# Optimization experiments

Hardware: AMD Instinct MI355X
Metric: run time of the kernel (lower is better)

Reference implementation:

```python
import jax, jax.numpy as jnp
import numpy as np

NUM_HEADS = 16
HEAD_DIM = 128
D_MODEL = 2048
SEQ = 2048
BATCH = 1


def setup_inputs() -> dict:
    key = jax.random.key(0)
    ks = jax.random.split(key, 7)
    s = 0.02
    return {
        "x": jax.random.normal(ks[0], (BATCH, SEQ, D_MODEL), dtype=jnp.float32),
        "q_w": jax.random.normal(ks[1], (D_MODEL, D_MODEL), dtype=jnp.float32) * s,
        "k_w": jax.random.normal(ks[2], (D_MODEL, D_MODEL), dtype=jnp.float32) * s,
        "v_w": jax.random.normal(ks[3], (D_MODEL, D_MODEL), dtype=jnp.float32) * s,
        "o_w": jax.random.normal(ks[4], (D_MODEL, D_MODEL), dtype=jnp.float32) * s,
        "gate_w": jax.random.normal(ks[5], (HEAD_DIM, HEAD_DIM), dtype=jnp.float32) * s,
        "gate_b": jax.random.normal(ks[6], (HEAD_DIM,), dtype=jnp.float32) * s,
    }


def reference(x, q_w, k_w, v_w, o_w, gate_w, gate_b):
    B, S, D = x.shape
    H, Hd = NUM_HEADS, HEAD_DIM
    # QKV projections (nn.Linear: y = x @ W^T), split into heads -> [B,H,S,Hd]
    def proj(w):
        return jnp.einsum('bsd,ed->bse', x, w).reshape(B, S, H, Hd).transpose(0, 2, 1, 3)
    q = proj(q_w)
    k = proj(k_w)
    v = proj(v_w)
    scale = 1.0 / jnp.sqrt(jnp.asarray(Hd, dtype=x.dtype))
    scores = jnp.einsum('bhqd,bhkd->bhqk', q, k) * scale  # [B,H,S,S]
    # causal mask
    causal = jnp.tril(jnp.ones((S, S), dtype=bool))
    scores = jnp.where(causal, scores, jnp.asarray(-1e30, dtype=scores.dtype))
    attn = jax.nn.softmax(scores, axis=-1)
    av = jnp.einsum('bhqk,bhkd->bhqd', attn, v)  # [B,H,S,Hd]
    # learned sigmoid gate computed from q, applied elementwise to attention output
    gate = jax.nn.sigmoid(jnp.einsum('bhqd,ed->bhqe', q, gate_w) + gate_b)
    out = av * gate
    out = out.transpose(0, 2, 1, 3).reshape(B, S, D)
    return jnp.einsum('bsd,ed->bse', out, o_w)
```

## Files before the change

### kernel.cpp

```cpp
#include <hip/hip_runtime.h>
#include <stdint.h>
#include <math.h>

#define DM 2048
#define NH 16
#define HD 128
#define LDQ (3 * DM)

typedef __bf16 bf16;
typedef __attribute__((ext_vector_type(8))) __bf16 bf16x8;
typedef __attribute__((ext_vector_type(4))) float f32x4;
typedef __attribute__((ext_vector_type(2))) unsigned int u32x2;

__device__ __forceinline__ void gload_lds16(const void* g, void* l) {
  __builtin_amdgcn_global_load_lds(
      (const __attribute__((address_space(1))) void*)g,
      (__attribute__((address_space(3))) void*)l,
      16, 0, 0);
}

__device__ __forceinline__ unsigned lds_addr(const void* p) {
  return (unsigned)(size_t)(const __attribute__((address_space(3))) void*)p;
}

template <int OFF>
__device__ __forceinline__ u32x2 tr_read(unsigned va) {
  u32x2 r;
  asm volatile("ds_read_b64_tr_b16 %0, %1 offset:%2"
               : "=v"(r) : "v"(va), "i"(OFF));
  return r;
}

#define TR4(dst, vd)                                        \
  dst[0] = tr_read<0>(vd);   dst[1] = tr_read<512>(vd);     \
  dst[2] = tr_read<1024>(vd); dst[3] = tr_read<1536>(vd);

__global__ __launch_bounds__(256) void cvt6(const float* xs, const float* qws,
                                            const float* kws, const float* vws,
                                            const float* ows, const float* gws,
                                            ushort* xd, ushort* w3d, ushort* owd,
                                            ushort* gwd) {
  const int y = blockIdx.y;
  const float4* s; ushort4* d; int n = (DM * DM) / 4;
  switch (y) {
    case 0: s = (const float4*)xs;  d = (ushort4*)xd;  break;
    case 1: s = (const float4*)qws; d = (ushort4*)w3d; break;
    case 2: s = (const float4*)kws; d = (ushort4*)(w3d + (size_t)DM * DM); break;
    case 3: s = (const float4*)vws; d = (ushort4*)(w3d + (size_t)2 * DM * DM); break;
    case 4: s = (const float4*)ows; d = (ushort4*)owd; break;
    default: s = (const float4*)gws; d = (ushort4*)gwd; n = (HD * HD) / 4; break;
  }
  int i = blockIdx.x * 256 + threadIdx.x;
  if (i >= n) return;
  float4 v = s[i];
  union { bf16 b[4]; ushort4 u; } r;
  r.b[0] = (bf16)v.x; r.b[1] = (bf16)v.y; r.b[2] = (bf16)v.z; r.b[3] = (bf16)v.w;
  d[i] = r.u;
}

__global__ __launch_bounds__(512, 2) void gemm_qkv(const bf16* __restrict__ A,
                                                   const bf16* __restrict__ Bw,
                                                   bf16* __restrict__ C) {
  __shared__ __align__(16) bf16 LA[2][256 * 64];
  __shared__ __align__(16) bf16 LB[2][192 * 64];
  const int tid = threadIdx.x;
  const int w = tid >> 6, l = tid & 63;
  const int wm = w >> 2, wn = w & 3;
  const int fr = l & 15, fg = l >> 4;
  const int bid = blockIdx.x;
  const int xcd = bid & 7, idx = bid >> 3;
  const int bm0 = (idx >> 2) * 256;
  const int bn0 = ((xcd << 2) | (idx & 3)) * 192;

  const int srow = l >> 3;
  const int sunit = (l & 7) ^ srow;
  const bf16* pa = A + (size_t)(bm0 + w * 32 + srow) * DM + sunit * 8;
  const bf16* pb = Bw + (size_t)(bn0 + w * 24 + srow) * DM + sunit * 8;

#define STG(buf, kt)                                                        \
  {                                                                         \
    _Pragma("unroll")                                                       \
    for (int i = 0; i < 4; i++)                                             \
      gload_lds16(pa + (size_t)i * 8 * DM + (kt) * 64,                      \
                  &LA[buf][(w * 32 + i * 8) * 64]);                         \
    _Pragma("unroll")                                                       \
    for (int i = 0; i < 3; i++)                                             \
      gload_lds16(pb + (size_t)i * 8 * DM + (kt) * 64,                      \
                  &LB[buf][(w * 24 + i * 8) * 64]);                         \
  }

  f32x4 acc[8][3] = {};

  STG(0, 0);
  STG(1, 1);
  asm volatile("s_waitcnt vmcnt(7)" ::: "memory");
  __builtin_amdgcn_s_barrier();

  const int sw0 = ((fg) ^ (fr & 7)) << 4;
  const int sw1 = ((4 + fg) ^ (fr & 7)) << 4;
  const char* AB = (const char*)&LA[0][0];
  const char* BB = (const char*)&LB[0][0];
  const int aoff = (wm * 128 + fr) * 128;
  const int boff = (wn * 48 + fr) * 128;

  bf16x8 bA[3], bB[3], aP[4], aQ[4], aR[4], aS[4];

#pragma unroll
  for (int n = 0; n < 3; n++) bA[n] = *(const bf16x8*)(BB + boff + n * 2048 + sw0);
#pragma unroll
  for (int m = 0; m < 4; m++) aP[m] = *(const bf16x8*)(AB + aoff + m * 2048 + sw0);
#pragma unroll
  for (int m = 0; m < 4; m++) aQ[m] = *(const bf16x8*)(AB + aoff + (m + 4) * 2048 + sw0);
  __builtin_amdgcn_sched_barrier(0);

  for (int t = 0; t < 32; ++t) {
    const int cur = t & 1;
    const char* Ac = AB + cur * 32768;
    const char* Bc = BB + cur * 24576;
#pragma unroll
    for (int n = 0; n < 3; n++) bB[n] = *(const bf16x8*)(Bc + boff + n * 2048 + sw1);
#pragma unroll
    for (int m = 0; m < 4; m++) aR[m] = *(const bf16x8*)(Ac + aoff + m * 2048 + sw1);
    asm volatile("s_waitcnt lgkmcnt(11)" ::: "memory");
    __builtin_amdgcn_sched_barrier(0);
    __builtin_amdgcn_s_setprio(1);
#pragma unroll
    for (int m = 0; m < 4; m++)
#pragma unroll
      for (int n = 0; n < 3; n++)
        acc[m][n] = __builtin_amdgcn_mfma_f32_16x16x32_bf16(aP[m], bA[n], acc[m][n], 0, 0, 0);
    __builtin_amdgcn_s_setprio(0);
    __builtin_amdgcn_sched_barrier(0);
#pragma unroll
    for (int m = 0; m < 4; m++) aS[m] = *(const bf16x8*)(Ac + aoff + (m + 4) * 2048 + sw1);
    asm volatile("s_waitcnt lgkmcnt(11)" ::: "memory");
    __builtin_amdgcn_sched_barrier(0);
    __builtin_amdgcn_s_setprio(1);
#pragma unroll
    for (int m = 0; m < 4; m++)
#pragma unroll
      for (int n = 0; n < 3; n++)
        acc[m + 4][n] = __builtin_amdgcn_mfma_f32_16x16x32_bf16(aQ[m], bA[n], acc[m + 4][n], 0, 0, 0);
    __builtin_amdgcn_s_setprio(0);
    __builtin_amdgcn_sched_barrier(0);
    asm volatile("s_waitcnt lgkmcnt(4)" ::: "memory");
    __builtin_amdgcn_sched_barrier(0);
    __builtin_amdgcn_s_setprio(1);
#pragma unroll
    for (int m = 0; m < 4; m++)
#pragma unroll
      for (int n = 0; n < 3; n++)
        acc[m][n] = __builtin_amdgcn_mfma_f32_16x16x32_bf16(aR[m], bB[n], acc[m][n], 0, 0, 0);
    __builtin_amdgcn_s_setprio(0);
    __builtin_amdgcn_sched_barrier(0);
    asm volatile("s_waitcnt lgkmcnt(0)" ::: "memory");
    __builtin_amdgcn_sched_barrier(0);
    __builtin_amdgcn_s_setprio(1);
#pragma unroll
    for (int m = 0; m < 4; m++)
#pragma unroll
      for (int n = 0; n < 3; n++)
        acc[m + 4][n] = __builtin_amdgcn_mfma_f32_16x16x32_bf16(aS[m], bB[n], acc[m + 4][n], 0, 0, 0);
    __builtin_amdgcn_s_setprio(0);
    __builtin_amdgcn_sched_barrier(0);

    __builtin_amdgcn_s_barrier();
    if (t < 30) {
      STG(cur, t + 2);
      asm volatile("s_waitcnt vmcnt(7)" ::: "memory");
    } else {
      asm volatile("s_waitcnt vmcnt(0)" ::: "memory");
    }
    __builtin_amdgcn_s_barrier();
    if (t < 31) {
      const char* An = AB + (cur ^ 1) * 32768;
      const char* Bn = BB + (cur ^ 1) * 24576;
#pragma unroll
      for (int n = 0; n < 3; n++) bA[n] = *(const bf16x8*)(Bn + boff + n * 2048 + sw0);
#pragma unroll
      for (int m = 0; m < 4; m++) aP[m] = *(const bf16x8*)(An + aoff + m * 2048 + sw0);
#pragma unroll
      for (int m = 0; m < 4; m++) aQ[m] = *(const bf16x8*)(An + aoff + (m + 4) * 2048 + sw0);
    }
    __builtin_amdgcn_sched_barrier(0);
  }

#pragma unroll
  for (int m = 0; m < 8; m++) {
    const int row0 = bm0 + wm * 128 + m * 16 + fg * 4;
#pragma unroll
    for (int n = 0; n < 3; n++) {
      const int col = bn0 + wn * 48 + n * 16 + fr;
#pragma unroll
      for (int j = 0; j < 4; j++) C[(size_t)(row0 + j) * LDQ + col] = (bf16)acc[m][n][j];
    }
  }
#undef STG
}

template <typename OutT>
__global__ __launch_bounds__(256) void gemm128(const bf16* __restrict__ A,
                                               const bf16* __restrict__ Bw,
                                               OutT* __restrict__ C, int ldc) {
  __shared__ __align__(16) bf16 As[128 * 32];
  __shared__ __align__(16) bf16 Bs[128 * 32];
  const int tid = threadIdx.x;
  const int w = tid >> 6, l = tid & 63;
  const int wr = w >> 1, wc = w & 1;
  const int bx = blockIdx.x, by = blockIdx.y;
  const int lrow = l >> 2, lcol = (l & 3) * 8;
  const int fr = l & 15, fg = l >> 4;
  const bf16* Ag = A + (size_t)(by * 128 + w * 32 + lrow) * DM + lcol;
  const bf16* Bg = Bw + (size_t)(bx * 128 + w * 32 + lrow) * DM + lcol;
  bf16* Asw = &As[(w * 32) * 32];
  bf16* Bsw = &Bs[(w * 32) * 32];
  f32x4 acc[4][4] = {};
  for (int kt = 0; kt < DM / 32; ++kt) {
    const int ko = kt * 32;
    gload_lds16(Ag + ko, Asw);
    gload_lds16(Ag + ko + 16 * DM, Asw + 16 * 32);
    gload_lds16(Bg + ko, Bsw);
    gload_lds16(Bg + ko + 16 * DM, Bsw + 16 * 32);
    __syncthreads();
    bf16x8 af[4], bfr[4];
#pragma unroll
    for (int m = 0; m < 4; m++)
      af[m] = *(const bf16x8*)&As[(wr * 64 + m * 16 + fr) * 32 + fg * 8];
#pragma unroll
    for (int n = 0; n < 4; n++)
      bfr[n] = *(const bf16x8*)&Bs[(wc * 64 + n * 16 + fr) * 32 + fg * 8];
#pragma unroll
    for (int m = 0; m < 4; m++)
#pragma unroll
      for (int n = 0; n < 4; n++)
        acc[m][n] = __builtin_amdgcn_mfma_f32_16x16x32_bf16(af[m], bfr[n], acc[m][n], 0, 0, 0);
    __syncthreads();
  }
#pragma unroll
  for (int m = 0; m < 4; m++) {
    const int row0 = by * 128 + wr * 64 + m * 16 + fg * 4;
#pragma unroll
    for (int n = 0; n < 4; n++) {
      const int col = bx * 128 + wc * 64 + n * 16 + fr;
#pragma unroll
      for (int j = 0; j < 4; j++) C[(size_t)(row0 + j) * ldc + col] = (OutT)acc[m][n][j];
    }
  }
}

__global__ __launch_bounds__(256, 2) void attn_k(const bf16* __restrict__ QKV,
                                                 const bf16* __restrict__ GWb,
                                                 const float* __restrict__ gbias,
                                                 bf16* __restrict__ Gout) {
  __shared__ __align__(16) bf16 Ks[2][8192];
  __shared__ __align__(16) bf16 Vs[2][8192];
  const int gid = blockIdx.x;
  const int h = gid & 15;
  const int idx = gid >> 4;
  const int qt = (idx < 16) ? (31 - idx) : (idx - 16);
  const int tid = threadIdx.x;
  const int w = tid >> 6, l = tid & 63;
  const int fr = l & 15, fg = l >> 4;
  const int fg4 = fg * 4;
  const int qbase = qt * 64 + w * 16;
  const int qg = qbase + fr;
  const int qcol = h * HD;
  const int kcol = DM + h * HD;
  const int vcol = 2 * DM + h * HD;
  const float scale = 0.08838834764831845f;

  bf16x8 bq[4];
#pragma unroll
  for (int kt = 0; kt < 4; kt++)
    bq[kt] = *(const bf16x8*)&QKV[(size_t)(qbase + fr) * LDQ + qcol + kt * 32 + fg * 8];

  const bf16* vbase = QKV + (size_t)(l >> 1) * LDQ + vcol + (l & 1) * 8;
  bf16* Ksl = &Ks[0][0];
  bf16* Vsl = &Vs[0][0];
  const unsigned ldsb = lds_addr(Vsl) + 8u * (unsigned)l;

#define STAGE(buf, kvbase)                                                    \
  {                                                                           \
    _Pragma("unroll")                                                         \
    for (int c = 0; c < 4; c++) {                                             \
      const int i = w * 4 + c;                                                \
      const int krow = i * 4 + (l >> 4);                                      \
      const int c16 = (l & 15) ^ (krow & 7);                                  \
      gload_lds16(QKV + (size_t)((kvbase) + krow) * LDQ + kcol + c16 * 8,     \
                  Ksl + (buf) * 8192 + i * 512);                              \
      const int db = i >> 1, k0 = (i & 1) * 32;                               \
      gload_lds16(vbase + (size_t)((kvbase) + k0) * LDQ + db * 16,            \
                  Vsl + (buf) * 8192 + db * 1024 + k0 * 16);                  \
    }                                                                         \
  }

  f32x4 oacc[8] = {};
  float m = -1e30f, lsum = 0.f;

  STAGE(0, 0);
  __syncthreads();

  for (int t = 0; t <= qt; ++t) {
    const int kv0 = t * 64;
    const int cur = t & 1;
    bf16x8 ak[4][4];
    {
      const char* Kb = (const char*)(Ksl + cur * 8192);
      const int swz = fr & 7;
#pragma unroll
      for (int kb = 0; kb < 4; kb++) {
        const char* rp = Kb + (kb * 16 + fr) * 256;
#pragma unroll
        for (int kt = 0; kt < 4; kt++)
          ak[kb][kt] = *(const bf16x8*)(rp + (((kt * 4 + fg) ^ swz) << 4));
      }
    }
    if (t < qt) STAGE(cur ^ 1, kv0 + 64);
    f32x4 sacc[4] = {};
#pragma unroll
    for (int kb = 0; kb < 4; kb++)
#pragma unroll
      for (int kt = 0; kt < 4; kt++)
        sacc[kb] = __builtin_amdgcn_mfma_f32_16x16x32_bf16(ak[kb][kt], bq[kt], sacc[kb], 0, 0, 0);
    const bool diag = (t == qt);
    float p[4][4];
    float tmax = -1e30f;
#pragma unroll
    for (int kb = 0; kb < 4; kb++)
#pragma unroll
      for (int j = 0; j < 4; j++) {
        float s = sacc[kb][j] * scale;
        if (diag && (kv0 + kb * 16 + fg4 + j) > qg) s = -1e30f;
        p[kb][j] = s;
        tmax = fmaxf(tmax, s);
      }
    tmax = fmaxf(tmax, __shfl_xor(tmax, 16, 64));
    tmax = fmaxf(tmax, __shfl_xor(tmax, 32, 64));
    const float mnew = fmaxf(m, tmax);
    const float alpha = __expf(m - mnew);
    m = mnew;
    float sum = 0.f;
#pragma unroll
    for (int kb = 0; kb < 4; kb++)
#pragma unroll
      for (int j = 0; j < 4; j++) {
        const float e = __expf(p[kb][j] - m);
        p[kb][j] = e;
        sum += e;
      }
    sum += __shfl_xor(sum, 16, 64);
    sum += __shfl_xor(sum, 32, 64);
    lsum = lsum * alpha + sum;
    float alpha4[4];
#pragma unroll
    for (int j = 0; j < 4; j++) alpha4[j] = __shfl(alpha, fg4 + j, 64);
#pragma unroll
    for (int db = 0; db < 8; db++)
#pragma unroll
      for (int j = 0; j < 4; j++) oacc[db][j] *= alpha4[j];
    bf16x8 pa[2];
#pragma unroll
    for (int kc = 0; kc < 2; kc++)
#pragma unroll
      for (int e = 0; e < 8; e++) pa[kc][e] = (bf16)p[2 * kc + (e >> 2)][e & 3];
    {
      const unsigned va = ldsb + (unsigned)cur * 16384u;
      u32x2 ta[4], tb[4];
      TR4(ta, va);
#pragma unroll
      for (int db = 0; db < 8; db++) {
        const u32x2* curp = (db & 1) ? tb : ta;
        u32x2* nxtp = (db & 1) ? ta : tb;
        if (db < 7) {
          const unsigned vd = va + (unsigned)(db + 1) * 2048u;
          TR4(nxtp, vd);
          asm volatile("s_waitcnt lgkmcnt(4)" ::: "memory");
        } else {
          asm volatile("s_waitcnt lgkmcnt(0)" ::: "memory");
        }
        __builtin_amdgcn_sched_barrier(0);
        union { u32x2 h[2]; bf16x8 v; } u0, u1;
        u0.h[0] = curp[0]; u0.h[1] = curp[1];
        u1.h[0] = curp[2]; u1.h[1] = curp[3];
        oacc[db] = __builtin_amdgcn_mfma_f32_16x16x32_bf16(pa[0], u0.v, oacc[db], 0, 0, 0);
        oacc[db] = __builtin_amdgcn_mfma_f32_16x16x32_bf16(pa[1], u1.v, oacc[db], 0, 0, 0);
      }
    }
    __syncthreads();
  }

  const float rinv = 1.0f / lsum;
  float rinv4[4];
#pragma unroll
  for (int j = 0; j < 4; j++) rinv4[j] = __shfl(rinv, fg4 + j, 64);
  f32x4 gacc[8] = {};
#pragma unroll
  for (int kt = 0; kt < 4; kt++)
#pragma unroll
    for (int eb = 0; eb < 8; eb++) {
      const bf16x8 bg = *(const bf16x8*)&GWb[(eb * 16 + fr) * HD + kt * 32 + fg * 8];
      gacc[eb] = __builtin_amdgcn_mfma_f32_16x16x32_bf16(bq[kt], bg, gacc[eb], 0, 0, 0);
    }
#pragma unroll
  for (int db = 0; db < 8; db++) {
    const int e = db * 16 + fr;
    const float bias = gbias[e];
    const int col = h * HD + e;
#pragma unroll
    for (int j = 0; j < 4; j++) {
      const float gate = 1.0f / (1.0f + __expf(-(gacc[db][j] + bias)));
      const float o = oacc[db][j] * rinv4[j] * gate;
      Gout[(size_t)(qbase + fg4 + j) * DM + col] = (bf16)o;
    }
  }
#undef STAGE
}

extern "C" void kernel_launch(void* const* d_in, const int* in_sizes, int n_in,
                              void* d_out, int out_size, void* d_ws, size_t ws_size,
                              hipStream_t stream) {
  const float* x  = (const float*)d_in[0];
  const float* qw = (const float*)d_in[1];
  const float* kw = (const float*)d_in[2];
  const float* vw = (const float*)d_in[3];
  const float* ow = (const float*)d_in[4];
  const float* gw = (const float*)d_in[5];
  const float* gb = (const float*)d_in[6];
  float* out = (float*)d_out;

  char* ws = (char*)d_ws;
  const size_t MB = 1024 * 1024;
  bf16* xb  = (bf16*)(ws + 0 * MB);
  bf16* w3b = (bf16*)(ws + 8 * MB);
  bf16* owb = (bf16*)(ws + 32 * MB);
  bf16* gwb = (bf16*)(ws + 40 * MB);
  bf16* QKV = (bf16*)(ws + 41 * MB);
  bf16* Gb  = (bf16*)(ws + 65 * MB);

  cvt6<<<dim3(4096, 6), 256, 0, stream>>>(x, qw, kw, vw, ow, gw,
                                          (ushort*)xb, (ushort*)w3b,
                                          (ushort*)owb, (ushort*)gwb);

  gemm_qkv<<<256, 512, 0, stream>>>(xb, w3b, QKV);

  attn_k<<<512, 256, 0, stream>>>(QKV, gwb, gb, Gb);

  gemm128<float><<<dim3(16, 16), 256, 0, stream>>>(Gb, owb, out, DM);
}
```

Baseline: 171.6 us.

## Triple-buffer K tiles and prefetch two tiles ahead in attention kernel

```diff
diff --git a/kernel.cpp b/kernel.cpp
--- a/kernel.cpp
+++ b/kernel.cpp
@@ -252,7 +252,7 @@
                                                  const bf16* __restrict__ GWb,
                                                  const float* __restrict__ gbias,
                                                  bf16* __restrict__ Gout) {
-  __shared__ __align__(16) bf16 Ks[2][8192];
+  __shared__ __align__(16) bf16 Ks[3][8192];
   __shared__ __align__(16) bf16 Vs[2][8192];
   const int gid = blockIdx.x;
   const int h = gid & 15;
@@ -275,11 +275,9 @@
     bq[kt] = *(const bf16x8*)&QKV[(size_t)(qbase + fr) * LDQ + qcol + kt * 32 + fg * 8];
 
   const bf16* vbase = QKV + (size_t)(l >> 1) * LDQ + vcol + (l & 1) * 8;
-  bf16* Ksl = &Ks[0][0];
-  bf16* Vsl = &Vs[0][0];
-  const unsigned ldsb = lds_addr(Vsl) + 8u * (unsigned)l;
-
-#define STAGE(buf, kvbase)                                                    \
+  const unsigned ldsb = lds_addr(&Vs[0][0]) + 8u * (unsigned)l;
+
+#define STAGE_K(buf, kvbase)                                                  \
   {                                                                           \
     _Pragma("unroll")                                                         \
     for (int c = 0; c < 4; c++) {                                             \
@@ -287,25 +285,45 @@
       const int krow = i * 4 + (l >> 4);                                      \
       const int c16 = (l & 15) ^ (krow & 7);                                  \
       gload_lds16(QKV + (size_t)((kvbase) + krow) * LDQ + kcol + c16 * 8,     \
-                  Ksl + (buf) * 8192 + i * 512);                              \
+                  &Ks[buf][i * 512]);                                         \
+    }                                                                         \
+  }
+#define STAGE_V(buf, kvbase)                                                  \
+  {                                                                           \
+    _Pragma("unroll")                                                         \
+    for (int c = 0; c < 4; c++) {                                             \
+      const int i = w * 4 + c;                                                \
       const int db = i >> 1, k0 = (i & 1) * 32;                               \
       gload_lds16(vbase + (size_t)((kvbase) + k0) * LDQ + db * 16,            \
-                  Vsl + (buf) * 8192 + db * 1024 + k0 * 16);                  \
+                  &Vs[buf][db * 1024 + k0 * 16]);                             \
     }                                                                         \
   }
 
   f32x4 oacc[8] = {};
   float m = -1e30f, lsum = 0.f;
 
-  STAGE(0, 0);
-  __syncthreads();
-
+  STAGE_K(0, 0);
+  STAGE_V(0, 0);
+  if (qt >= 1) {
+    STAGE_K(1, 64);
+    asm volatile("s_waitcnt vmcnt(4)" ::: "memory");
+  } else {
+    asm volatile("s_waitcnt vmcnt(0)" ::: "memory");
+  }
+  __builtin_amdgcn_sched_barrier(0);
+  __builtin_amdgcn_s_barrier();
+  __builtin_amdgcn_sched_barrier(0);
+
+  int kc = 0;
   for (int t = 0; t <= qt; ++t) {
     const int kv0 = t * 64;
-    const int cur = t & 1;
+    if (t + 1 <= qt) STAGE_V((t + 1) & 1, kv0 + 64);
+    const int kc2 = (kc == 0) ? 2 : (kc - 1);
+    if (t + 2 <= qt) STAGE_K(kc2, kv0 + 128);
+
     bf16x8 ak[4][4];
     {
-      const char* Kb = (const char*)(Ksl + cur * 8192);
+      const char* Kb = (const char*)&Ks[kc][0];
       const int swz = fr & 7;
 #pragma unroll
       for (int kb = 0; kb < 4; kb++) {
@@ -315,7 +333,6 @@
           ak[kb][kt] = *(const bf16x8*)(rp + (((kt * 4 + fg) ^ swz) << 4));
       }
     }
-    if (t < qt) STAGE(cur ^ 1, kv0 + 64);
     f32x4 sacc[4] = {};
 #pragma unroll
     for (int kb = 0; kb < 4; kb++)
@@ -360,11 +377,11 @@
       for (int j = 0; j < 4; j++) oacc[db][j] *= alpha4[j];
     bf16x8 pa[2];
 #pragma unroll
-    for (int kc = 0; kc < 2; kc++)
-#pragma unroll
-      for (int e = 0; e < 8; e++) pa[kc][e] = (bf16)p[2 * kc + (e >> 2)][e & 3];
+    for (int kc8 = 0; kc8 < 2; kc8++)
+#pragma unroll
+      for (int e = 0; e < 8; e++) pa[kc8][e] = (bf16)p[2 * kc8 + (e >> 2)][e & 3];
     {
-      const unsigned va = ldsb + (unsigned)cur * 16384u;
+      const unsigned va = ldsb + (unsigned)(t & 1) * 16384u;
       u32x2 ta[4], tb[4];
       TR4(ta, va);
 #pragma unroll
@@ -386,7 +403,17 @@
         oacc[db] = __builtin_amdgcn_mfma_f32_16x16x32_bf16(pa[1], u1.v, oacc[db], 0, 0, 0);
       }
     }
-    __syncthreads();
+    if (t < qt) {
+      if (t + 2 <= qt) {
+        asm volatile("s_waitcnt vmcnt(4)" ::: "memory");
+      } else {
+        asm volatile("s_waitcnt vmcnt(0)" ::: "memory");
+      }
+      __builtin_amdgcn_sched_barrier(0);
+      __builtin_amdgcn_s_barrier();
+      __builtin_amdgcn_sched_barrier(0);
+    }
+    kc = (kc == 2) ? 0 : kc + 1;
   }
 
   const float rinv = 1.0f / lsum;
@@ -413,7 +440,8 @@
       Gout[(size_t)(qbase + fg4 + j) * DM + col] = (bf16)o;
     }
   }
-#undef STAGE
+#undef STAGE_K
+#undef STAGE_V
 }
 
 extern "C" void kernel_launch(void* const* d_in, const int* in_sizes, int n_in,
```

New measurement: 184.2 us. 1.07x slower.

## Split causal attention along the KV axis into chunked partials with a merge kernel

Applied to the files above, without the earlier changes.

```diff
diff --git a/kernel.cpp b/kernel.cpp
--- a/kernel.cpp
+++ b/kernel.cpp
@@ -248,16 +248,22 @@
   }
 }
 
-__global__ __launch_bounds__(256, 2) void attn_k(const bf16* __restrict__ QKV,
-                                                 const bf16* __restrict__ GWb,
-                                                 const float* __restrict__ gbias,
-                                                 bf16* __restrict__ Gout) {
+__global__ __launch_bounds__(256, 2) void attn_p1(const bf16* __restrict__ QKV,
+                                                  bf16* __restrict__ Opart,
+                                                  float* __restrict__ ml) {
   __shared__ __align__(16) bf16 Ks[2][8192];
   __shared__ __align__(16) bf16 Vs[2][8192];
   const int gid = blockIdx.x;
   const int h = gid & 15;
-  const int idx = gid >> 4;
-  const int qt = (idx < 16) ? (31 - idx) : (idx - 16);
+  const int c = 79 - (gid >> 4);
+  int qt, ch;
+  if (c < 8)       { qt = c;                ch = 0; }
+  else if (c < 24) { int r = c - 8;  qt = 8 + (r >> 1);  ch = r & 1; }
+  else if (c < 48) { int r = c - 24; int q3 = r / 3; qt = 16 + q3; ch = r - 3 * q3; }
+  else             { int r = c - 48; qt = 24 + (r >> 2); ch = r & 3; }
+  const int t0 = ch * 8;
+  const int t1 = min(t0 + 8, qt + 1);
+
   const int tid = threadIdx.x;
   const int w = tid >> 6, l = tid & 63;
   const int fr = l & 15, fg = l >> 4;
@@ -282,8 +288,8 @@
 #define STAGE(buf, kvbase)                                                    \
   {                                                                           \
     _Pragma("unroll")                                                         \
-    for (int c = 0; c < 4; c++) {                                             \
-      const int i = w * 4 + c;                                                \
+    for (int cc = 0; cc < 4; cc++) {                                          \
+      const int i = w * 4 + cc;                                               \
       const int krow = i * 4 + (l >> 4);                                      \
       const int c16 = (l & 15) ^ (krow & 7);                                  \
       gload_lds16(QKV + (size_t)((kvbase) + krow) * LDQ + kcol + c16 * 8,     \
@@ -297,12 +303,12 @@
   f32x4 oacc[8] = {};
   float m = -1e30f, lsum = 0.f;
 
-  STAGE(0, 0);
+  STAGE(0, t0 * 64);
   __syncthreads();
 
-  for (int t = 0; t <= qt; ++t) {
+  for (int t = t0; t < t1; ++t) {
     const int kv0 = t * 64;
-    const int cur = t & 1;
+    const int cur = (t - t0) & 1;
     bf16x8 ak[4][4];
     {
       const char* Kb = (const char*)(Ksl + cur * 8192);
@@ -315,7 +321,7 @@
           ak[kb][kt] = *(const bf16x8*)(rp + (((kt * 4 + fg) ^ swz) << 4));
       }
     }
-    if (t < qt) STAGE(cur ^ 1, kv0 + 64);
+    if (t + 1 < t1) STAGE(cur ^ 1, kv0 + 64);
     f32x4 sacc[4] = {};
 #pragma unroll
     for (int kb = 0; kb < 4; kb++)
@@ -360,9 +366,9 @@
       for (int j = 0; j < 4; j++) oacc[db][j] *= alpha4[j];
     bf16x8 pa[2];
 #pragma unroll
-    for (int kc = 0; kc < 2; kc++)
-#pragma unroll
-      for (int e = 0; e < 8; e++) pa[kc][e] = (bf16)p[2 * kc + (e >> 2)][e & 3];
+    for (int kc8 = 0; kc8 < 2; kc8++)
+#pragma unroll
+      for (int e = 0; e < 8; e++) pa[kc8][e] = (bf16)p[2 * kc8 + (e >> 2)][e & 3];
     {
       const unsigned va = ldsb + (unsigned)cur * 16384u;
       u32x2 ta[4], tb[4];
@@ -379,9 +385,9 @@
           asm volatile("s_waitcnt lgkmcnt(0)" ::: "memory");
         }
         __builtin_amdgcn_sched_barrier(0);
-        union { u32x2 h[2]; bf16x8 v; } u0, u1;
-        u0.h[0] = curp[0]; u0.h[1] = curp[1];
-        u1.h[0] = curp[2]; u1.h[1] = curp[3];
+        union { u32x2 h2[2]; bf16x8 v; } u0, u1;
+        u0.h2[0] = curp[0]; u0.h2[1] = curp[1];
+        u1.h2[0] = curp[2]; u1.h2[1] = curp[3];
         oacc[db] = __builtin_amdgcn_mfma_f32_16x16x32_bf16(pa[0], u0.v, oacc[db], 0, 0, 0);
         oacc[db] = __builtin_amdgcn_mfma_f32_16x16x32_bf16(pa[1], u1.v, oacc[db], 0, 0, 0);
       }
@@ -389,10 +395,41 @@
     __syncthreads();
   }
 
-  const float rinv = 1.0f / lsum;
-  float rinv4[4];
-#pragma unroll
-  for (int j = 0; j < 4; j++) rinv4[j] = __shfl(rinv, fg4 + j, 64);
+  const int slot = h * 128 + qt * 4 + ch;
+  bf16* Op = Opart + (size_t)slot * 8192;
+#pragma unroll
+  for (int db = 0; db < 8; db++)
+#pragma unroll
+    for (int j = 0; j < 4; j++)
+      Op[(w * 16 + fg4 + j) * 128 + db * 16 + fr] = (bf16)oacc[db][j];
+  if (fg == 0) {
+    ml[slot * 128 + w * 16 + fr] = m;
+    ml[slot * 128 + 64 + w * 16 + fr] = lsum;
+  }
+#undef STAGE
+}
+
+__global__ __launch_bounds__(256) void attn_p2(const bf16* __restrict__ QKV,
+                                               const bf16* __restrict__ Opart,
+                                               const float* __restrict__ ml,
+                                               const bf16* __restrict__ GWb,
+                                               const float* __restrict__ gbias,
+                                               bf16* __restrict__ Gout) {
+  const int qt = blockIdx.x;
+  const int h = blockIdx.y;
+  const int nch = (qt >> 3) + 1;
+  const int slot0 = h * 128 + qt * 4;
+  const int tid = threadIdx.x;
+  const int w = tid >> 6, l = tid & 63;
+  const int fr = l & 15, fg = l >> 4;
+  const int fg4 = fg * 4;
+  const int qbase = qt * 64 + w * 16;
+
+  bf16x8 bq[4];
+#pragma unroll
+  for (int kt = 0; kt < 4; kt++)
+    bq[kt] = *(const bf16x8*)&QKV[(size_t)(qbase + fr) * LDQ + h * HD + kt * 32 + fg * 8];
+
   f32x4 gacc[8] = {};
 #pragma unroll
   for (int kt = 0; kt < 4; kt++)
@@ -401,6 +438,28 @@
       const bf16x8 bg = *(const bf16x8*)&GWb[(eb * 16 + fr) * HD + kt * 32 + fg * 8];
       gacc[eb] = __builtin_amdgcn_mfma_f32_16x16x32_bf16(bq[kt], bg, gacc[eb], 0, 0, 0);
     }
+
+  float wgt[4][4];
+#pragma unroll
+  for (int j = 0; j < 4; j++) {
+    const int row = w * 16 + fg4 + j;
+    float mi[4], li[4];
+    float mmax = -1e30f;
+    for (int i = 0; i < nch; i++) {
+      mi[i] = ml[(slot0 + i) * 128 + row];
+      li[i] = ml[(slot0 + i) * 128 + 64 + row];
+      mmax = fmaxf(mmax, mi[i]);
+    }
+    float den = 0.f;
+    for (int i = 0; i < nch; i++) {
+      const float e = __expf(mi[i] - mmax);
+      wgt[j][i] = e;
+      den += li[i] * e;
+    }
+    const float rinv = 1.0f / den;
+    for (int i = 0; i < nch; i++) wgt[j][i] *= rinv;
+  }
+
 #pragma unroll
   for (int db = 0; db < 8; db++) {
     const int e = db * 16 + fr;
@@ -408,12 +467,14 @@
     const int col = h * HD + e;
 #pragma unroll
     for (int j = 0; j < 4; j++) {
+      const int row = w * 16 + fg4 + j;
+      float o = 0.f;
+      for (int i = 0; i < nch; i++)
+        o += (float)Opart[(size_t)(slot0 + i) * 8192 + row * 128 + e] * wgt[j][i];
       const float gate = 1.0f / (1.0f + __expf(-(gacc[db][j] + bias)));
-      const float o = oacc[db][j] * rinv4[j] * gate;
-      Gout[(size_t)(qbase + fg4 + j) * DM + col] = (bf16)o;
-    }
-  }
-#undef STAGE
+      Gout[(size_t)(qbase + fg4 + j) * DM + col] = (bf16)(o * gate);
+    }
+  }
 }
 
 extern "C" void kernel_launch(void* const* d_in, const int* in_sizes, int n_in,
@@ -430,12 +491,14 @@
 
   char* ws = (char*)d_ws;
   const size_t MB = 1024 * 1024;
-  bf16* xb  = (bf16*)(ws + 0 * MB);
-  bf16* w3b = (bf16*)(ws + 8 * MB);
-  bf16* owb = (bf16*)(ws + 32 * MB);
-  bf16* gwb = (bf16*)(ws + 40 * MB);
-  bf16* QKV = (bf16*)(ws + 41 * MB);
-  bf16* Gb  = (bf16*)(ws + 65 * MB);
+  bf16* xb   = (bf16*)(ws + 0 * MB);
+  bf16* w3b  = (bf16*)(ws + 8 * MB);
+  bf16* Opart= (bf16*)(ws + 0 * MB);
+  bf16* owb  = (bf16*)(ws + 32 * MB);
+  bf16* gwb  = (bf16*)(ws + 40 * MB);
+  bf16* QKV  = (bf16*)(ws + 41 * MB);
+  bf16* Gb   = (bf16*)(ws + 65 * MB);
+  float* mlb = (float*)(ws + 73 * MB);
 
   cvt6<<<dim3(4096, 6), 256, 0, stream>>>(x, qw, kw, vw, ow, gw,
                                           (ushort*)xb, (ushort*)w3b,
@@ -443,7 +506,8 @@
 
   gemm_qkv<<<256, 512, 0, stream>>>(xb, w3b, QKV);
 
-  attn_k<<<512, 256, 0, stream>>>(QKV, gwb, gb, Gb);
+  attn_p1<<<1280, 256, 0, stream>>>(QKV, Opart, mlb);
+  attn_p2<<<dim3(32, 16), 256, 0, stream>>>(QKV, Opart, mlb, gwb, gb, Gb);
 
   gemm128<float><<<dim3(16, 16), 256, 0, stream>>>(Gb, owb, out, DM);
 }
```

Measured after the change: 206.5 us. 1.2x slower.

## Single-buffer K/V shared tiles and raise attention occupancy to four blocks

Applied to the files above, without the earlier changes.

```diff
diff --git a/kernel.cpp b/kernel.cpp
--- a/kernel.cpp
+++ b/kernel.cpp
@@ -248,12 +248,12 @@
   }
 }
 
-__global__ __launch_bounds__(256, 2) void attn_k(const bf16* __restrict__ QKV,
+__global__ __launch_bounds__(256, 4) void attn_k(const bf16* __restrict__ QKV,
                                                  const bf16* __restrict__ GWb,
                                                  const float* __restrict__ gbias,
                                                  bf16* __restrict__ Gout) {
-  __shared__ __align__(16) bf16 Ks[2][8192];
-  __shared__ __align__(16) bf16 Vs[2][8192];
+  __shared__ __align__(16) bf16 Ks[8192];
+  __shared__ __align__(16) bf16 Vs[8192];
   const int gid = blockIdx.x;
   const int h = gid & 15;
   const int idx = gid >> 4;
@@ -275,11 +275,9 @@
     bq[kt] = *(const bf16x8*)&QKV[(size_t)(qbase + fr) * LDQ + qcol + kt * 32 + fg * 8];
 
   const bf16* vbase = QKV + (size_t)(l >> 1) * LDQ + vcol + (l & 1) * 8;
-  bf16* Ksl = &Ks[0][0];
-  bf16* Vsl = &Vs[0][0];
-  const unsigned ldsb = lds_addr(Vsl) + 8u * (unsigned)l;
-
-#define STAGE(buf, kvbase)                                                    \
+  const unsigned ldsb = lds_addr(&Vs[0]) + 8u * (unsigned)l;
+
+#define STAGE(kvbase)                                                         \
   {                                                                           \
     _Pragma("unroll")                                                         \
     for (int c = 0; c < 4; c++) {                                             \
@@ -287,25 +285,24 @@
       const int krow = i * 4 + (l >> 4);                                      \
       const int c16 = (l & 15) ^ (krow & 7);                                  \
       gload_lds16(QKV + (size_t)((kvbase) + krow) * LDQ + kcol + c16 * 8,     \
-                  Ksl + (buf) * 8192 + i * 512);                              \
+                  &Ks[i * 512]);                                              \
       const int db = i >> 1, k0 = (i & 1) * 32;                               \
       gload_lds16(vbase + (size_t)((kvbase) + k0) * LDQ + db * 16,            \
-                  Vsl + (buf) * 8192 + db * 1024 + k0 * 16);                  \
+                  &Vs[db * 1024 + k0 * 16]);                                  \
     }                                                                         \
   }
 
   f32x4 oacc[8] = {};
   float m = -1e30f, lsum = 0.f;
 
-  STAGE(0, 0);
+  STAGE(0);
   __syncthreads();
 
   for (int t = 0; t <= qt; ++t) {
     const int kv0 = t * 64;
-    const int cur = t & 1;
     bf16x8 ak[4][4];
     {
-      const char* Kb = (const char*)(Ksl + cur * 8192);
+      const char* Kb = (const char*)&Ks[0];
       const int swz = fr & 7;
 #pragma unroll
       for (int kb = 0; kb < 4; kb++) {
@@ -315,7 +312,6 @@
           ak[kb][kt] = *(const bf16x8*)(rp + (((kt * 4 + fg) ^ swz) << 4));
       }
     }
-    if (t < qt) STAGE(cur ^ 1, kv0 + 64);
     f32x4 sacc[4] = {};
 #pragma unroll
     for (int kb = 0; kb < 4; kb++)
@@ -364,7 +360,7 @@
 #pragma unroll
       for (int e = 0; e < 8; e++) pa[kc][e] = (bf16)p[2 * kc + (e >> 2)][e & 3];
     {
-      const unsigned va = ldsb + (unsigned)cur * 16384u;
+      const unsigned va = ldsb;
       u32x2 ta[4], tb[4];
       TR4(ta, va);
 #pragma unroll
@@ -379,14 +375,18 @@
           asm volatile("s_waitcnt lgkmcnt(0)" ::: "memory");
         }
         __builtin_amdgcn_sched_barrier(0);
-        union { u32x2 h[2]; bf16x8 v; } u0, u1;
-        u0.h[0] = curp[0]; u0.h[1] = curp[1];
-        u1.h[0] = curp[2]; u1.h[1] = curp[3];
+        union { u32x2 h2[2]; bf16x8 v; } u0, u1;
+        u0.h2[0] = curp[0]; u0.h2[1] = curp[1];
+        u1.h2[0] = curp[2]; u1.h2[1] = curp[3];
         oacc[db] = __builtin_amdgcn_mfma_f32_16x16x32_bf16(pa[0], u0.v, oacc[db], 0, 0, 0);
         oacc[db] = __builtin_amdgcn_mfma_f32_16x16x32_bf16(pa[1], u1.v, oacc[db], 0, 0, 0);
       }
     }
-    __syncthreads();
+    if (t < qt) {
+      __syncthreads();
+      STAGE(kv0 + 64);
+      __syncthreads();
+    }
   }
 
   const float rinv = 1.0f / lsum;
```

New measurement: 192.4 us. 1.12x slower.
